# Performance work log

Hardware: AMD Instinct MI355X
Metric: run time of the kernel (lower is better)

Reference implementation:

```python
import jax, jax.numpy as jnp
import numpy as np


def setup_inputs() -> dict:
    key = jax.random.key(0)
    ks = jax.random.split(key, 7)
    B, C, N, E = 2, 64, 1024, 32
    s = float(np.sqrt(2.0) / 2.0)
    return {
        "emb": jax.random.normal(ks[0], (B, C, N), dtype=jnp.float32),
        "th12_1": jax.random.uniform(ks[1], (E, C), minval=-s, maxval=s, dtype=jnp.float32),
        "th34_1": jax.random.uniform(ks[2], (E, C), minval=-s, maxval=s, dtype=jnp.float32),
        "th5_1": jax.random.uniform(ks[3], (E,), minval=-s, maxval=s, dtype=jnp.float32),
        "th12_2": jax.random.uniform(ks[4], (E, C), minval=-s, maxval=s, dtype=jnp.float32),
        "th34_2": jax.random.uniform(ks[5], (E, C), minval=-s, maxval=s, dtype=jnp.float32),
        "th5_2": jax.random.uniform(ks[6], (E,), minval=-s, maxval=s, dtype=jnp.float32),
    }


def _node2edge(emb, th12, th5):
    # emb: (B, C, N); th12: (E, C); th5: (E,)
    N = emb.shape[-1]
    t = jnp.einsum('ec,bcn->ben', th12, emb)  # (B, E, N)
    # pairwise max over (i, j); NOTE original returns 2*max + theta5*I (sum_thx unused)
    m = jnp.maximum(t[:, :, :, None], t[:, :, None, :])  # (B, E, N, N)
    eye = jnp.eye(N, dtype=emb.dtype)
    return jax.nn.relu(m + m + th5[None, :, None, None] * eye[None, None])


def reference(emb, th12_1, th34_1, th5_1, th12_2, th34_2, th5_2):
    adj = _node2edge(emb, th12_1, th5_1)
    gate = jax.nn.sigmoid(_node2edge(emb, th12_2, th5_2))
    return adj * gate
```

## Files before the change

### kernel.cpp

```cpp
#include <hip/hip_runtime.h>

#define B_DIM 2
#define C_DIM 64
#define N_DIM 1024
#define E_DIM 32
#define BE_DIM (B_DIM * E_DIM)
#define ITILE 16

#define RCP_LN2  1.4426950408889634f
#define TWO_RCP_LN2 2.8853900817779268f

typedef float f32x4 __attribute__((ext_vector_type(4)));

__global__ __launch_bounds__(256) void compute_t_kernel(
    const float* __restrict__ emb,
    const float* __restrict__ th12_1,
    const float* __restrict__ th12_2,
    float* __restrict__ t1,
    float* __restrict__ t2)
{
    const int n  = blockIdx.x * 256 + threadIdx.x;
    const int be = blockIdx.y;
    const int b  = be >> 5;
    const int e  = be & 31;

    const float* __restrict__ embp = emb + (size_t)b * C_DIM * N_DIM + n;
    const float* __restrict__ w1   = th12_1 + e * C_DIM;
    const float* __restrict__ w2   = th12_2 + e * C_DIM;

    float acc1 = 0.f, acc2 = 0.f;
#pragma unroll
    for (int c = 0; c < C_DIM; ++c) {
        const float x = embp[(size_t)c * N_DIM];
        acc1 = fmaf(w1[c], x, acc1);
        acc2 = fmaf(w2[c], x, acc2);
    }
    t1[be * N_DIM + n] = acc1;
    t2[be * N_DIM + n] = acc2;
}

__global__ __launch_bounds__(256) void edge_kernel(
    const float* __restrict__ t1,
    const float* __restrict__ t2,
    const float* __restrict__ th5_1,
    const float* __restrict__ th5_2,
    float* __restrict__ out)
{
    const int be = blockIdx.y;
    const int e  = be & (E_DIM - 1);
    const int i0 = blockIdx.x * ITILE;
    const int jb = threadIdx.x * 4;

    const float* __restrict__ t1r = t1 + be * N_DIM;
    const float* __restrict__ t2r = t2 + be * N_DIM;

    const float th51  = th5_1[e];
    const float th52s = th5_2[e] * RCP_LN2;

    const f32x4 a = *reinterpret_cast<const f32x4*>(t1r + jb);
    const f32x4 g = *reinterpret_cast<const f32x4*>(t2r + jb);

    const float a2[4] = {a.x + a.x, a.y + a.y, a.z + a.z, a.w + a.w};
    const float gs[4] = {g.x * TWO_RCP_LN2, g.y * TWO_RCP_LN2,
                         g.z * TWO_RCP_LN2, g.w * TWO_RCP_LN2};

    float t1i2[ITILE], t2is[ITILE];
#pragma unroll
    for (int r = 0; r < ITILE; ++r) {
        t1i2[r] = 2.f * t1r[i0 + r];
        t2is[r] = TWO_RCP_LN2 * t2r[i0 + r];
    }

    float* dst = out + ((size_t)be * N_DIM + i0) * N_DIM + jb;

#pragma unroll
    for (int r = 0; r < ITILE; ++r) {
        const int i = i0 + r;

        f32x4 o;
#pragma unroll
        for (int k = 0; k < 4; ++k) {
            const float adj = fmaxf(fmaxf(t1i2[r], a2[k]), 0.f);
            const float y   = fmaxf(fmaxf(t2is[r], gs[k]), 0.f);
            const float gate = __builtin_amdgcn_rcpf(1.f + exp2f(-y));
            o[k] = adj * gate;
        }

        const int kd = i - jb;
        if ((unsigned)kd < 4u) {
            const float adjd = fmaxf(t1i2[r] + th51, 0.f);
            const float yd   = fmaxf(t2is[r] + th52s, 0.f);
            const float dv   = adjd * __builtin_amdgcn_rcpf(1.f + exp2f(-yd));
            o[kd] = dv;
        }

        __builtin_nontemporal_store(o,
            reinterpret_cast<f32x4*>(dst + (size_t)r * N_DIM));
    }
}

extern "C" void kernel_launch(void* const* d_in, const int* in_sizes, int n_in,
                              void* d_out, int out_size, void* d_ws, size_t ws_size,
                              hipStream_t stream) {
    const float* emb    = (const float*)d_in[0];
    const float* th12_1 = (const float*)d_in[1];
    const float* th5_1  = (const float*)d_in[3];
    const float* th12_2 = (const float*)d_in[4];
    const float* th5_2  = (const float*)d_in[6];
    float* out = (float*)d_out;

    float* t1 = (float*)d_ws;
    float* t2 = t1 + (size_t)BE_DIM * N_DIM;

    dim3 g1(N_DIM / 256, BE_DIM);
    compute_t_kernel<<<g1, 256, 0, stream>>>(emb, th12_1, th12_2, t1, t2);

    dim3 g2(N_DIM / ITILE, BE_DIM);
    edge_kernel<<<g2, 256, 0, stream>>>(t1, t2, th5_1, th5_2, out);
}
```

Baseline: 283.5 us.

## Fuse projection into edge kernel and share row values via LDS

Merges the channel projection kernel into the pairwise edge kernel: each block recomputes the t1/t2 projections for its column slice from emb, and the 16 row values are exchanged through shared memory. This removes the second launch and the workspace round trip. In exchange, every row-tile block redundantly recomputes the 64-channel projection and rereads emb from cache, and a barrier is added.

```diff
diff --git a/kernel.cpp b/kernel.cpp
--- a/kernel.cpp
+++ b/kernel.cpp
@@ -7,69 +7,62 @@
 #define BE_DIM (B_DIM * E_DIM)
 #define ITILE 16
 
-#define RCP_LN2  1.4426950408889634f
+#define RCP_LN2     1.4426950408889634f
 #define TWO_RCP_LN2 2.8853900817779268f
 
 typedef float f32x4 __attribute__((ext_vector_type(4)));
 
-__global__ __launch_bounds__(256) void compute_t_kernel(
+__global__ __launch_bounds__(256) void fused_kernel(
     const float* __restrict__ emb,
     const float* __restrict__ th12_1,
     const float* __restrict__ th12_2,
-    float* __restrict__ t1,
-    float* __restrict__ t2)
-{
-    const int n  = blockIdx.x * 256 + threadIdx.x;
-    const int be = blockIdx.y;
-    const int b  = be >> 5;
-    const int e  = be & 31;
-
-    const float* __restrict__ embp = emb + (size_t)b * C_DIM * N_DIM + n;
-    const float* __restrict__ w1   = th12_1 + e * C_DIM;
-    const float* __restrict__ w2   = th12_2 + e * C_DIM;
-
-    float acc1 = 0.f, acc2 = 0.f;
-#pragma unroll
-    for (int c = 0; c < C_DIM; ++c) {
-        const float x = embp[(size_t)c * N_DIM];
-        acc1 = fmaf(w1[c], x, acc1);
-        acc2 = fmaf(w2[c], x, acc2);
-    }
-    t1[be * N_DIM + n] = acc1;
-    t2[be * N_DIM + n] = acc2;
-}
-
-__global__ __launch_bounds__(256) void edge_kernel(
-    const float* __restrict__ t1,
-    const float* __restrict__ t2,
     const float* __restrict__ th5_1,
     const float* __restrict__ th5_2,
     float* __restrict__ out)
 {
     const int be = blockIdx.y;
+    const int b  = be >> 5;
     const int e  = be & (E_DIM - 1);
     const int i0 = blockIdx.x * ITILE;
     const int jb = threadIdx.x * 4;
 
-    const float* __restrict__ t1r = t1 + be * N_DIM;
-    const float* __restrict__ t2r = t2 + be * N_DIM;
+    const float* __restrict__ embp = emb + (size_t)b * C_DIM * N_DIM + jb;
+    const float* __restrict__ w1   = th12_1 + e * C_DIM;
+    const float* __restrict__ w2   = th12_2 + e * C_DIM;
 
-    const float th51  = th5_1[e];
-    const float th52s = th5_2[e] * RCP_LN2;
+    f32x4 acc1 = {0.f, 0.f, 0.f, 0.f};
+    f32x4 acc2 = {0.f, 0.f, 0.f, 0.f};
+#pragma unroll 16
+    for (int c = 0; c < C_DIM; ++c) {
+        const f32x4 x = *reinterpret_cast<const f32x4*>(embp + (size_t)c * N_DIM);
+        acc1 += w1[c] * x;
+        acc2 += w2[c] * x;
+    }
 
-    const f32x4 a = *reinterpret_cast<const f32x4*>(t1r + jb);
-    const f32x4 g = *reinterpret_cast<const f32x4*>(t2r + jb);
+    const f32x4 a2 = acc1 + acc1;
+    const f32x4 gs = acc2 * TWO_RCP_LN2;
 
-    const float a2[4] = {a.x + a.x, a.y + a.y, a.z + a.z, a.w + a.w};
-    const float gs[4] = {g.x * TWO_RCP_LN2, g.y * TWO_RCP_LN2,
-                         g.z * TWO_RCP_LN2, g.w * TWO_RCP_LN2};
+    __shared__ float t1i2_lds[ITILE];
+    __shared__ float t2is_lds[ITILE];
+    const int rel = jb - i0;
+    if ((unsigned)rel < (unsigned)ITILE) {
+#pragma unroll
+        for (int k = 0; k < 4; ++k) {
+            t1i2_lds[rel + k] = a2[k];
+            t2is_lds[rel + k] = gs[k];
+        }
+    }
+    __syncthreads();
 
     float t1i2[ITILE], t2is[ITILE];
 #pragma unroll
     for (int r = 0; r < ITILE; ++r) {
-        t1i2[r] = 2.f * t1r[i0 + r];
-        t2is[r] = TWO_RCP_LN2 * t2r[i0 + r];
+        t1i2[r] = t1i2_lds[r];
+        t2is[r] = t2is_lds[r];
     }
+
+    const float th51  = th5_1[e];
+    const float th52s = th5_2[e] * RCP_LN2;
 
     float* dst = out + ((size_t)be * N_DIM + i0) * N_DIM + jb;
 
@@ -80,8 +73,8 @@
         f32x4 o;
 #pragma unroll
         for (int k = 0; k < 4; ++k) {
-            const float adj = fmaxf(fmaxf(t1i2[r], a2[k]), 0.f);
-            const float y   = fmaxf(fmaxf(t2is[r], gs[k]), 0.f);
+            const float adj  = fmaxf(fmaxf(t1i2[r], a2[k]), 0.f);
+            const float y    = fmaxf(fmaxf(t2is[r], gs[k]), 0.f);
             const float gate = __builtin_amdgcn_rcpf(1.f + exp2f(-y));
             o[k] = adj * gate;
         }
@@ -90,8 +83,7 @@
         if ((unsigned)kd < 4u) {
             const float adjd = fmaxf(t1i2[r] + th51, 0.f);
             const float yd   = fmaxf(t2is[r] + th52s, 0.f);
-            const float dv   = adjd * __builtin_amdgcn_rcpf(1.f + exp2f(-yd));
-            o[kd] = dv;
+            o[kd] = adjd * __builtin_amdgcn_rcpf(1.f + exp2f(-yd));
         }
 
         __builtin_nontemporal_store(o,
@@ -108,13 +100,8 @@
     const float* th12_2 = (const float*)d_in[4];
     const float* th5_2  = (const float*)d_in[6];
     float* out = (float*)d_out;
+    (void)d_ws; (void)ws_size;
 
-    float* t1 = (float*)d_ws;
-    float* t2 = t1 + (size_t)BE_DIM * N_DIM;
-
-    dim3 g1(N_DIM / 256, BE_DIM);
-    compute_t_kernel<<<g1, 256, 0, stream>>>(emb, th12_1, th12_2, t1, t2);
-
-    dim3 g2(N_DIM / ITILE, BE_DIM);
-    edge_kernel<<<g2, 256, 0, stream>>>(t1, t2, th5_1, th5_2, out);
+    dim3 g(N_DIM / ITILE, BE_DIM);
+    fused_kernel<<<g, 256, 0, stream>>>(emb, th12_1, th12_2, th5_1, th5_2, out);
 }
```

Result: slower. 291.8 us (+2.9%).
